# Kernel optimization log

Measured on AMD Instinct MI355X. Metric: run time of the kernel, lower is better.

Reference implementation:

```python
import jax, jax.numpy as jnp
import numpy as np

N_USERS = 100000
N_ITEMS = 50000
N_LAYERS = 3
LATENT_DIM = 64
N_INTERACTIONS = 600000
BATCH = 4096
N_TOTAL = N_USERS + N_ITEMS


def setup_inputs() -> dict:
    key = jax.random.key(0)
    k_e, k_u, k_p, k_n = jax.random.split(key, 4)

    # --- build bipartite interaction graph (numpy, host-side like scipy in the original) ---
    rng = np.random.default_rng(0)
    u = rng.integers(0, N_USERS, size=N_INTERACTIONS)
    i = rng.integers(0, N_ITEMS, size=N_INTERACTIONS) + N_USERS
    # symmetrize: A[u, i] = 1 and A[i, u] = 1
    row = np.concatenate([u, i]).astype(np.int32)
    col = np.concatenate([i, u]).astype(np.int32)
    # symmetric degree normalization: D^{-1/2} A D^{-1/2}
    deg = np.bincount(row, minlength=N_TOTAL).astype(np.float32)
    d_inv = np.power(deg + 1e-9, -0.5)
    d_inv[np.isinf(d_inv)] = 0.0
    vals = (d_inv[row] * d_inv[col]).astype(np.float32)

    # Xavier-uniform init for E0 (fan_in = fan_out = dims of the weight matrix)
    limit = float(np.sqrt(6.0 / (N_TOTAL + LATENT_DIM)))
    E0 = jax.random.uniform(k_e, (N_TOTAL, LATENT_DIM), jnp.float32, -limit, limit)

    return {
        "users": jax.random.randint(k_u, (BATCH,), 0, N_USERS),
        "pos_items": jax.random.randint(k_p, (BATCH,), 0, N_ITEMS),
        "neg_items": jax.random.randint(k_n, (BATCH,), 0, N_ITEMS),
        "E0": E0,
        "adj_row": jnp.asarray(row),
        "adj_col": jnp.asarray(col),
        "adj_vals": jnp.asarray(vals),
    }


def reference(users, pos_items, neg_items, E0, adj_row, adj_col, adj_vals):
    # SpMM via gather + segment-sum: out[r] = sum_{e: row[e]=r} vals[e] * E[col[e]]
    def spmm(E):
        return jax.ops.segment_sum(adj_vals[:, None] * E[adj_col], adj_row,
                                   num_segments=N_TOTAL)

    # layer propagation with running sum (mean over layer stack)
    E_k = E0
    acc = E0
    for _ in range(N_LAYERS):
        E_k = spmm(E_k)
        acc = acc + E_k
    final_emb = acc / (N_LAYERS + 1)  # [N_TOTAL, D]

    user_emb = final_emb[:N_USERS]
    item_emb = final_emb[N_USERS:]

    u_emb = user_emb[users]
    pos_emb = item_emb[pos_items]
    neg_emb = item_emb[neg_items]
    u_emb0 = E0[users]
    pos_emb0 = E0[N_USERS + pos_items]
    neg_emb0 = E0[N_USERS + neg_items]
    return (u_emb, pos_emb, neg_emb, u_emb0, pos_emb0, neg_emb0)
```

## Files before the change

kernel.cpp:

```cpp
#include <hip/hip_runtime.h>
#include <hip/hip_fp16.h>

#define LATENT 64
#define N_USERS_C 100000

#define BROWS 128
#define LOG_BROWS 7
#define NBUCK_MAX 1280
#define NBLKA_MAX 512
#define SORT_T 256
#define SORT_E 16
#define SORT_CHUNK (SORT_T * SORT_E)
#define BUCK_CAP 4608

__device__ __forceinline__ unsigned enc_val14(float v) {
    unsigned vb = (unsigned)__float_as_int(v) + 0x1000u;
    return (((vb >> 23) - 0x77u) << 10) | ((vb >> 13) & 0x3FFu);
}
__device__ __forceinline__ float dec_val14(unsigned m) {
    return __uint_as_float(m ? ((((m >> 10) + 0x77u) << 23) | ((m & 0x3FFu) << 13)) : 0u);
}


__global__ void sortA_kernel(const int* __restrict__ row, const int* __restrict__ col,
                             const float* __restrict__ vals,
                             unsigned* __restrict__ aux, unsigned char* __restrict__ rowloc,
                             int* __restrict__ cntmat, int* __restrict__ srcmat,
                             int* __restrict__ bcnt, int nnz, int nbuck) {
    __shared__ int cnt[NBUCK_MAX];
    __shared__ int off[NBUCK_MAX];
    __shared__ int part[SORT_T];
    __shared__ unsigned buf[SORT_CHUNK];
    __shared__ unsigned char rbuf[SORT_CHUNK];
    int t = threadIdx.x, blk = blockIdx.x;
    int base = blk * SORT_CHUNK;

    for (int i = t; i < nbuck; i += SORT_T) cnt[i] = 0;
    __syncthreads();

    int      eb[SORT_E];
    unsigned pl[SORT_E];
    unsigned char rl8[SORT_E];
#pragma unroll
    for (int j = 0; j < SORT_E; j++) {
        int e = base + j * SORT_T + t;
        if (e < nnz) {
            int r = row[e];
            int b = r >> LOG_BROWS;
            eb[j] = b;
            pl[j] = (unsigned)col[e] | (enc_val14(vals[e]) << 18);
            rl8[j] = (unsigned char)(r & (BROWS - 1));
            atomicAdd(&cnt[b], 1);
        } else {
            eb[j] = -1;
        }
    }
    __syncthreads();

    int chunk = (nbuck + SORT_T - 1) / SORT_T;
    int lo = t * chunk, hi = lo + chunk; if (hi > nbuck) hi = nbuck;
    int s = 0;
    for (int i = lo; i < hi; i++) s += cnt[i];
    part[t] = s;
    __syncthreads();
    for (int o = 1; o < SORT_T; o <<= 1) {
        int x = (t >= o) ? part[t - o] : 0;
        __syncthreads();
        part[t] += x;
        __syncthreads();
    }
    int run = (t == 0) ? 0 : part[t - 1];
    for (int i = lo; i < hi; i++) { off[i] = run; run += cnt[i]; }
    __syncthreads();

#pragma unroll
    for (int j = 0; j < SORT_E; j++) {
        if (eb[j] >= 0) {
            int p = atomicAdd(&off[eb[j]], 1);
            buf[p] = pl[j];
            rbuf[p] = rl8[j];
        }
    }
    __syncthreads();

    for (int b = t; b < nbuck; b += SORT_T) {
        int c = cnt[b];
        int beg = off[b] - c;
        cntmat[(size_t)blk * nbuck + b] = c;
        srcmat[(size_t)blk * nbuck + b] = beg;
        if (c) atomicAdd(&bcnt[b], c);
    }
    int nvalid = nnz - base; if (nvalid > SORT_CHUNK) nvalid = SORT_CHUNK;
    for (int i = t; i < nvalid; i += SORT_T) {
        aux[base + i] = buf[i];
        rowloc[base + i] = rbuf[i];
    }
}


__global__ void bscan_kernel(const int* __restrict__ bcnt, int* __restrict__ bstart,
                             int nbuck) {
    __shared__ int part[SORT_T];
    int t = threadIdx.x;
    int chunk = (nbuck + SORT_T - 1) / SORT_T;
    int lo = t * chunk, hi = lo + chunk; if (hi > nbuck) hi = nbuck;
    int s = 0;
    for (int i = lo; i < hi; i++) s += bcnt[i];
    part[t] = s;
    __syncthreads();
    for (int o = 1; o < SORT_T; o <<= 1) {
        int x = (t >= o) ? part[t - o] : 0;
        __syncthreads();
        part[t] += x;
        __syncthreads();
    }
    int run = (t == 0) ? 0 : part[t - 1];
    for (int i = lo; i < hi; i++) { bstart[i] = run; run += bcnt[i]; }
    if (t == SORT_T - 1) bstart[nbuck] = run;
}


__global__ void sortB_kernel(const unsigned* __restrict__ aux,
                             const unsigned char* __restrict__ rowloc,
                             const int* __restrict__ cntmat, const int* __restrict__ srcmat,
                             const int* __restrict__ bstart,
                             unsigned* __restrict__ edges, int* __restrict__ startOut,
                             int* __restrict__ origRow, int* __restrict__ slotOfRow,
                             int nblkA, int nbuck, int ntotal, int nnz) {
    __shared__ int rs[NBLKA_MAX], roff[NBLKA_MAX + 1];
    __shared__ int part[SORT_T];
    __shared__ unsigned buf[BUCK_CAP];
    __shared__ unsigned char rbuf[BUCK_CAP];
    __shared__ int cnt128[BROWS];
    __shared__ int slotOf[BROWS];
    __shared__ int rowOf[BROWS];
    __shared__ int offS[BROWS];
    __shared__ int placeOff[BROWS];
    __shared__ int dhist[64];
    int b = blockIdx.x, t = threadIdx.x;
    int base = bstart[b];
    int tot = bstart[b + 1] - base;
    int rbase = b * BROWS;
    int nr = ntotal - rbase; if (nr > BROWS) nr = BROWS;

    int chunk = (nblkA + SORT_T - 1) / SORT_T;
    int lo = t * chunk, hi = lo + chunk; if (hi > nblkA) hi = nblkA;
    int rcl[8];
    int s = 0;
    for (int i = lo; i < hi; i++) {
        int c = cntmat[(size_t)i * nbuck + b];
        rcl[i - lo] = c;
        rs[i] = srcmat[(size_t)i * nbuck + b];
        s += c;
    }
    part[t] = s;
    if (t < BROWS) cnt128[t] = 0;
    if (t < 64) dhist[t] = 0;
    __syncthreads();
    for (int o = 1; o < SORT_T; o <<= 1) {
        int x = (t >= o) ? part[t - o] : 0;
        __syncthreads();
        part[t] += x;
        __syncthreads();
    }
    int run = (t == 0) ? 0 : part[t - 1];
    for (int i = lo; i < hi; i++) { roff[i] = run; run += rcl[i - lo]; }
    if (t == SORT_T - 1) roff[nblkA] = part[SORT_T - 1];
    __syncthreads();

    for (int i = t; i < tot; i += SORT_T) {
        int lo2 = 0, hi2 = nblkA;
        while (hi2 - lo2 > 1) {
            int mid = (lo2 + hi2) >> 1;
            if (roff[mid] <= i) lo2 = mid; else hi2 = mid;
        }
        size_t src = (size_t)lo2 * SORT_CHUNK + rs[lo2] + (i - roff[lo2]);
        buf[i] = aux[src];
        unsigned char rl = rowloc[src];
        rbuf[i] = rl;
        atomicAdd(&cnt128[rl], 1);
    }
    __syncthreads();

    if (t < nr) { int d = min(cnt128[t], 63); atomicAdd(&dhist[d], 1); }
    __syncthreads();
    part[t] = (t < 64) ? dhist[t] : 0;
    __syncthreads();
    for (int o = 1; o < 64; o <<= 1) {
        int x = (t >= o) ? part[t - o] : 0;
        __syncthreads();
        part[t] += x;
        __syncthreads();
    }
    if (t < 64) dhist[t] = (t == 0) ? 0 : part[t - 1];
    __syncthreads();
    if (t < nr) {
        int d = min(cnt128[t], 63);
        int sl = atomicAdd(&dhist[d], 1);
        slotOf[t] = sl;
        rowOf[sl] = t;
    }
    __syncthreads();

    part[t] = (t < nr) ? cnt128[rowOf[t]] : 0;
    __syncthreads();
    for (int o = 1; o < SORT_T; o <<= 1) {
        int x = (t >= o) ? part[t - o] : 0;
        __syncthreads();
        part[t] += x;
        __syncthreads();
    }
    if (t < nr) offS[t] = (t == 0) ? 0 : part[t - 1];
    __syncthreads();

    if (t < nr) {
        startOut[rbase + t]   = base + offS[t];
        origRow[rbase + t]    = rbase + rowOf[t];
        slotOfRow[rbase + t]  = rbase + slotOf[t];
        placeOff[t] = offS[slotOf[t]];
    }
    if (b == nbuck - 1 && t == 0) startOut[ntotal] = nnz;
    __syncthreads();

    for (int i = t; i < tot; i += SORT_T) {
        int p = atomicAdd(&placeOff[rbuf[i]], 1);
        edges[base + p] = buf[i];
    }
}

__global__ void conv_kernel(const float* __restrict__ in, __half* __restrict__ outh, int n4) {
    int i = blockIdx.x * blockDim.x + threadIdx.x;
    if (i >= n4) return;
    float4 v = ((const float4*)in)[i];
    __half2* o = (__half2*)outh;
    o[2 * i]     = __floats2half2_rn(v.x, v.y);
    o[2 * i + 1] = __floats2half2_rn(v.z, v.w);
}


__global__ void spmm_slot(const int* __restrict__ start, const int* __restrict__ origRow,
                          const unsigned* __restrict__ edges,
                          const __half* __restrict__ Ein, __half* __restrict__ Eout,
                          int nslots) {
    int t = blockIdx.x * blockDim.x + threadIdx.x;
    int w = t >> 6;
    int lane = t & 63;
    int g = lane >> 4, l = lane & 15;
    int s = 4 * w + g;
    if (s >= nslots) return;
    int b = start[s];
    int e = start[s + 1];
    int ro = origRow[s];
    float a0 = 0.f, a1 = 0.f, a2 = 0.f, a3 = 0.f;
    for (int k = b; k < e; k += 4) {
        unsigned ed[4];
#pragma unroll
        for (int j = 0; j < 4; j++) {
            int kk = k + j;
            ed[j] = (kk < e) ? edges[kk] : 0u;
        }
        ushort4 gv[4];
#pragma unroll
        for (int j = 0; j < 4; j++) {
            gv[j] = *(const ushort4*)(Ein + (size_t)(ed[j] & 0x3FFFFu) * LATENT + 4 * l);
        }
#pragma unroll
        for (int j = 0; j < 4; j++) {
            float wv = dec_val14(ed[j] >> 18);
            const __half2* h2 = (const __half2*)&gv[j];
            a0 += wv * __low2float(h2[0]);
            a1 += wv * __high2float(h2[0]);
            a2 += wv * __low2float(h2[1]);
            a3 += wv * __high2float(h2[1]);
        }
    }
    union { ushort4 u; __half2 h[2]; } o;
    o.h[0] = __floats2half2_rn(a0, a1);
    o.h[1] = __floats2half2_rn(a2, a3);
    *(ushort4*)(Eout + (size_t)ro * LATENT + 4 * l) = o.u;
}


__global__ void fin_fused(const int* __restrict__ users, const int* __restrict__ pos,
                          const int* __restrict__ neg,
                          const int* __restrict__ start, const int* __restrict__ slotOfRow,
                          const unsigned* __restrict__ edges,
                          const float* __restrict__ E0, const __half* __restrict__ E1,
                          const __half* __restrict__ E2,
                          float* __restrict__ out, int batch) {
    int t = blockIdx.x * blockDim.x + threadIdx.x;
    int w = t >> 6;
    int lane = t & 63;
    int g = lane >> 4, l = lane & 15;
    int i = 4 * w + g;
    int nent = 3 * batch;
    if (i >= nent) return;
    int grp = i / batch;
    int bb = i - grp * batch;
    int r = (grp == 0) ? users[bb] : (grp == 1) ? (N_USERS_C + pos[bb]) : (N_USERS_C + neg[bb]);
    int s = slotOfRow[r];
    int b = start[s];
    int e = start[s + 1];
    float a0 = 0.f, a1 = 0.f, a2 = 0.f, a3 = 0.f;
    for (int k = b; k < e; k += 4) {
        unsigned ed[4];
#pragma unroll
        for (int j = 0; j < 4; j++) {
            int kk = k + j;
            ed[j] = (kk < e) ? edges[kk] : 0u;
        }
        ushort4 gv[4];
#pragma unroll
        for (int j = 0; j < 4; j++) {
            gv[j] = *(const ushort4*)(E2 + (size_t)(ed[j] & 0x3FFFFu) * LATENT + 4 * l);
        }
#pragma unroll
        for (int j = 0; j < 4; j++) {
            float wv = dec_val14(ed[j] >> 18);
            const __half2* h2 = (const __half2*)&gv[j];
            a0 += wv * __low2float(h2[0]);
            a1 += wv * __high2float(h2[0]);
            a2 += wv * __low2float(h2[1]);
            a3 += wv * __high2float(h2[1]);
        }
    }
    size_t idx = (size_t)r * LATENT + 4 * l;
    float4 e0v = *(const float4*)(E0 + idx);
    ushort4 e1u = *(const ushort4*)(E1 + idx);
    ushort4 e2u = *(const ushort4*)(E2 + idx);
    const __half2* h1 = (const __half2*)&e1u;
    const __half2* h2v = (const __half2*)&e2u;
    float4 res;
    res.x = 0.25f * (e0v.x + __low2float(h1[0])  + __low2float(h2v[0])  + a0);
    res.y = 0.25f * (e0v.y + __high2float(h1[0]) + __high2float(h2v[0]) + a1);
    res.z = 0.25f * (e0v.z + __low2float(h1[1])  + __low2float(h2v[1])  + a2);
    res.w = 0.25f * (e0v.w + __high2float(h1[1]) + __high2float(h2v[1]) + a3);
    int total = nent * LATENT;
    *(float4*)(out + (size_t)i * LATENT + 4 * l) = res;
    *(float4*)(out + total + (size_t)i * LATENT + 4 * l) = e0v;
}

extern "C" void kernel_launch(void* const* d_in, const int* in_sizes, int n_in,
                              void* d_out, int out_size, void* d_ws, size_t ws_size,
                              hipStream_t stream) {
    const int*   users = (const int*)d_in[0];
    const int*   pos   = (const int*)d_in[1];
    const int*   neg   = (const int*)d_in[2];
    const float* E0    = (const float*)d_in[3];
    const int*   row   = (const int*)d_in[4];
    const int*   col   = (const int*)d_in[5];
    const float* vals  = (const float*)d_in[6];
    float*       out   = (float*)d_out;

    const int batch  = in_sizes[0];
    const int nnz    = in_sizes[4];
    const int ntotal = in_sizes[3] / LATENT;
    const int nbuck  = (ntotal + BROWS - 1) / BROWS;
    const int nblkA  = (nnz + SORT_CHUNK - 1) / SORT_CHUNK;

    auto align256 = [](size_t x) { return (x + 255) & ~(size_t)255; };

    const size_t hbufBytes = align256((size_t)ntotal * LATENT * sizeof(__half));
    const size_t edgeBytes = align256((size_t)nnz * sizeof(unsigned));
    const size_t auxBytes  = align256((size_t)nnz * sizeof(unsigned));
    const size_t matBytes  = align256((size_t)nblkA * nbuck * sizeof(int));
    const size_t stBytes   = align256((size_t)(ntotal + 1) * sizeof(int));
    const size_t bsBytes   = align256((size_t)(nbuck + 1) * sizeof(int));

    char* p = (char*)d_ws;
    __half* E0h      = (__half*)p;          p += hbufBytes;
    __half* bufA     = (__half*)p;          p += hbufBytes;
    __half* bufB     = (__half*)p;          p += hbufBytes;
    __half* bufC     = (__half*)p;          p += hbufBytes;
    unsigned* edges  = (unsigned*)p;        p += edgeBytes;
    int*    startA   = (int*)p;             p += stBytes;
    int*    origRow  = (int*)p;             p += stBytes;
    int*    slotOfRw = (int*)p;             p += stBytes;
    int*    bstart   = (int*)p;             p += bsBytes;
    int*    bcnt     = (int*)p;             p += bsBytes;
    unsigned*      aux    = (unsigned*)bufC;
    unsigned char* rowloc = (unsigned char*)((char*)bufC + auxBytes);
    int* cntmat = (int*)bufB;
    int* srcmat = (int*)((char*)bufB + matBytes);

    hipMemsetAsync(bcnt, 0, (size_t)nbuck * sizeof(int), stream);

    const int threads = 256;
    const int slotWaves = (ntotal + 3) / 4;
    const int spBlocks = (slotWaves * 64 + threads - 1) / threads;
    const int nent = 3 * batch;
    const int fBlocks = (((nent + 3) / 4) * 64 + threads - 1) / threads;
    const int n4 = ntotal * LATENT / 4;
    const int cBlocks = (n4 + threads - 1) / threads;

    sortA_kernel<<<nblkA, SORT_T, 0, stream>>>(row, col, vals, aux, rowloc,
                                               cntmat, srcmat, bcnt, nnz, nbuck);
    bscan_kernel<<<1, SORT_T, 0, stream>>>(bcnt, bstart, nbuck);
    conv_kernel<<<cBlocks, threads, 0, stream>>>(E0, E0h, n4);
    sortB_kernel<<<nbuck, SORT_T, 0, stream>>>(aux, rowloc, cntmat, srcmat, bstart,
                                               edges, startA, origRow, slotOfRw,
                                               nblkA, nbuck, ntotal, nnz);

    spmm_slot<<<spBlocks, threads, 0, stream>>>(startA, origRow, edges, E0h, bufA, ntotal);
    spmm_slot<<<spBlocks, threads, 0, stream>>>(startA, origRow, edges, bufA, bufB, ntotal);
    fin_fused<<<fBlocks, threads, 0, stream>>>(users, pos, neg, startA, slotOfRw, edges,
                                               E0, bufA, bufB, out, batch);
}
```

Measured before the change: 204.7 us.

## Fold bucket scan into sortB, fp16 conversion into sortA, unroll gathers by 8

Removes the single-block bucket-scan launch: each sortB block now computes its own bucket base with a block-wide prefix sum over bcnt. Moves the E0 fp32-to-fp16 conversion into sortA as a grid-stride loop, dropping a separate launch. Widens the SpMM edge-gather unroll from 4 to 8 to keep more loads in flight. In exchange, every sortB block redoes the scan, and the wider unroll raises register pressure and wastes lanes on rows with few edges.

```diff
diff --git a/kernel.cpp b/kernel.cpp
--- a/kernel.cpp
+++ b/kernel.cpp
@@ -26,7 +26,9 @@
                              const float* __restrict__ vals,
                              unsigned* __restrict__ aux, unsigned char* __restrict__ rowloc,
                              int* __restrict__ cntmat, int* __restrict__ srcmat,
-                             int* __restrict__ bcnt, int nnz, int nbuck) {
+                             int* __restrict__ bcnt,
+                             const float* __restrict__ E0, __half* __restrict__ E0h,
+                             int n4, int nnz, int nbuck) {
     __shared__ int cnt[NBUCK_MAX];
     __shared__ int off[NBUCK_MAX];
     __shared__ int part[SORT_T];
@@ -95,35 +97,21 @@
         aux[base + i] = buf[i];
         rowloc[base + i] = rbuf[i];
     }
-}
-
-
-__global__ void bscan_kernel(const int* __restrict__ bcnt, int* __restrict__ bstart,
-                             int nbuck) {
-    __shared__ int part[SORT_T];
-    int t = threadIdx.x;
-    int chunk = (nbuck + SORT_T - 1) / SORT_T;
-    int lo = t * chunk, hi = lo + chunk; if (hi > nbuck) hi = nbuck;
-    int s = 0;
-    for (int i = lo; i < hi; i++) s += bcnt[i];
-    part[t] = s;
-    __syncthreads();
-    for (int o = 1; o < SORT_T; o <<= 1) {
-        int x = (t >= o) ? part[t - o] : 0;
-        __syncthreads();
-        part[t] += x;
-        __syncthreads();
-    }
-    int run = (t == 0) ? 0 : part[t - 1];
-    for (int i = lo; i < hi; i++) { bstart[i] = run; run += bcnt[i]; }
-    if (t == SORT_T - 1) bstart[nbuck] = run;
+
+    int stride = gridDim.x * SORT_T;
+    for (int i = blk * SORT_T + t; i < n4; i += stride) {
+        float4 v = ((const float4*)E0)[i];
+        __half2* o = (__half2*)E0h;
+        o[2 * i]     = __floats2half2_rn(v.x, v.y);
+        o[2 * i + 1] = __floats2half2_rn(v.z, v.w);
+    }
 }
 
 
 __global__ void sortB_kernel(const unsigned* __restrict__ aux,
                              const unsigned char* __restrict__ rowloc,
                              const int* __restrict__ cntmat, const int* __restrict__ srcmat,
-                             const int* __restrict__ bstart,
+                             const int* __restrict__ bcnt,
                              unsigned* __restrict__ edges, int* __restrict__ startOut,
                              int* __restrict__ origRow, int* __restrict__ slotOfRow,
                              int nblkA, int nbuck, int ntotal, int nnz) {
@@ -137,11 +125,29 @@
     __shared__ int offS[BROWS];
     __shared__ int placeOff[BROWS];
     __shared__ int dhist[64];
+    __shared__ int baseSh;
     int b = blockIdx.x, t = threadIdx.x;
-    int base = bstart[b];
-    int tot = bstart[b + 1] - base;
     int rbase = b * BROWS;
     int nr = ntotal - rbase; if (nr > BROWS) nr = BROWS;
+
+    {
+        int chunkB = (nbuck + SORT_T - 1) / SORT_T;
+        int loB = t * chunkB, hiB = loB + chunkB; if (hiB > nbuck) hiB = nbuck;
+        int sB = 0;
+        for (int i = loB; i < hiB && i < b; i++) sB += bcnt[i];
+        part[t] = sB;
+        __syncthreads();
+        for (int o = 1; o < SORT_T; o <<= 1) {
+            int x = (t >= o) ? part[t - o] : 0;
+            __syncthreads();
+            part[t] += x;
+            __syncthreads();
+        }
+        if (t == SORT_T - 1) baseSh = part[SORT_T - 1];
+        __syncthreads();
+    }
+    int base = baseSh;
+    int tot = bcnt[b];
 
     int chunk = (nblkA + SORT_T - 1) / SORT_T;
     int lo = t * chunk, hi = lo + chunk; if (hi > nblkA) hi = nblkA;
@@ -226,15 +232,6 @@
         int p = atomicAdd(&placeOff[rbuf[i]], 1);
         edges[base + p] = buf[i];
     }
-}
-
-__global__ void conv_kernel(const float* __restrict__ in, __half* __restrict__ outh, int n4) {
-    int i = blockIdx.x * blockDim.x + threadIdx.x;
-    if (i >= n4) return;
-    float4 v = ((const float4*)in)[i];
-    __half2* o = (__half2*)outh;
-    o[2 * i]     = __floats2half2_rn(v.x, v.y);
-    o[2 * i + 1] = __floats2half2_rn(v.z, v.w);
 }
 
 
@@ -252,20 +249,20 @@
     int e = start[s + 1];
     int ro = origRow[s];
     float a0 = 0.f, a1 = 0.f, a2 = 0.f, a3 = 0.f;
-    for (int k = b; k < e; k += 4) {
-        unsigned ed[4];
-#pragma unroll
-        for (int j = 0; j < 4; j++) {
+    for (int k = b; k < e; k += 8) {
+        unsigned ed[8];
+#pragma unroll
+        for (int j = 0; j < 8; j++) {
             int kk = k + j;
             ed[j] = (kk < e) ? edges[kk] : 0u;
         }
-        ushort4 gv[4];
-#pragma unroll
-        for (int j = 0; j < 4; j++) {
+        ushort4 gv[8];
+#pragma unroll
+        for (int j = 0; j < 8; j++) {
             gv[j] = *(const ushort4*)(Ein + (size_t)(ed[j] & 0x3FFFFu) * LATENT + 4 * l);
         }
 #pragma unroll
-        for (int j = 0; j < 4; j++) {
+        for (int j = 0; j < 8; j++) {
             float wv = dec_val14(ed[j] >> 18);
             const __half2* h2 = (const __half2*)&gv[j];
             a0 += wv * __low2float(h2[0]);
@@ -302,20 +299,20 @@
     int b = start[s];
     int e = start[s + 1];
     float a0 = 0.f, a1 = 0.f, a2 = 0.f, a3 = 0.f;
-    for (int k = b; k < e; k += 4) {
-        unsigned ed[4];
-#pragma unroll
-        for (int j = 0; j < 4; j++) {
+    for (int k = b; k < e; k += 8) {
+        unsigned ed[8];
+#pragma unroll
+        for (int j = 0; j < 8; j++) {
             int kk = k + j;
             ed[j] = (kk < e) ? edges[kk] : 0u;
         }
-        ushort4 gv[4];
-#pragma unroll
-        for (int j = 0; j < 4; j++) {
+        ushort4 gv[8];
+#pragma unroll
+        for (int j = 0; j < 8; j++) {
             gv[j] = *(const ushort4*)(E2 + (size_t)(ed[j] & 0x3FFFFu) * LATENT + 4 * l);
         }
 #pragma unroll
-        for (int j = 0; j < 4; j++) {
+        for (int j = 0; j < 8; j++) {
             float wv = dec_val14(ed[j] >> 18);
             const __half2* h2 = (const __half2*)&gv[j];
             a0 += wv * __low2float(h2[0]);
@@ -376,7 +373,6 @@
     int*    startA   = (int*)p;             p += stBytes;
     int*    origRow  = (int*)p;             p += stBytes;
     int*    slotOfRw = (int*)p;             p += stBytes;
-    int*    bstart   = (int*)p;             p += bsBytes;
     int*    bcnt     = (int*)p;             p += bsBytes;
     unsigned*      aux    = (unsigned*)bufC;
     unsigned char* rowloc = (unsigned char*)((char*)bufC + auxBytes);
@@ -391,13 +387,11 @@
     const int nent = 3 * batch;
     const int fBlocks = (((nent + 3) / 4) * 64 + threads - 1) / threads;
     const int n4 = ntotal * LATENT / 4;
-    const int cBlocks = (n4 + threads - 1) / threads;
 
     sortA_kernel<<<nblkA, SORT_T, 0, stream>>>(row, col, vals, aux, rowloc,
-                                               cntmat, srcmat, bcnt, nnz, nbuck);
-    bscan_kernel<<<1, SORT_T, 0, stream>>>(bcnt, bstart, nbuck);
-    conv_kernel<<<cBlocks, threads, 0, stream>>>(E0, E0h, n4);
-    sortB_kernel<<<nbuck, SORT_T, 0, stream>>>(aux, rowloc, cntmat, srcmat, bstart,
+                                               cntmat, srcmat, bcnt,
+                                               E0, E0h, n4, nnz, nbuck);
+    sortB_kernel<<<nbuck, SORT_T, 0, stream>>>(aux, rowloc, cntmat, srcmat, bcnt,
                                                edges, startA, origRow, slotOfRw,
                                                nblkA, nbuck, ntotal, nnz);
 
```

New measurement: 211.7 us. +3.4%, slower.
